# Optimization experiments

Measured on AMD Instinct MI355X. Metric: run time of the kernel, lower is better.

## Reference

```python
import jax, jax.numpy as jnp
import numpy as np

B, T, NUM_SKILLS, CONCEPT_NUM, HIDDEN = 64, 200, 1024, 256, 1024


def setup_inputs() -> dict:
    key = jax.random.key(0)
    ks = jax.random.split(key, 12)
    s_in = 1.0 / np.sqrt(NUM_SKILLS)
    s_h = 1.0 / np.sqrt(HIDDEN)
    s_c = 1.0 / np.sqrt(CONCEPT_NUM)
    return {
        "q_hot": jax.random.normal(ks[0], (B, T, NUM_SKILLS), jnp.float32),
        "result": jax.random.randint(ks[1], (B, T), 0, 2, jnp.int32),
        "next_q_hot": jax.random.normal(ks[2], (B, T, NUM_SKILLS), jnp.float32),
        "concept_num": CONCEPT_NUM,
        # kc: Linear(num_skills -> concept_num)
        "W_kc": jax.random.uniform(ks[3], (CONCEPT_NUM, NUM_SKILLS), jnp.float32, -s_in, s_in),
        "b_kc": jax.random.uniform(ks[4], (CONCEPT_NUM,), jnp.float32, -s_in, s_in),
        # LSTM (input = 2*concept_num, hidden = HIDDEN), torch gate order i,f,g,o
        "W_ih": jax.random.uniform(ks[5], (4 * HIDDEN, 2 * CONCEPT_NUM), jnp.float32, -s_h, s_h),
        "W_hh": jax.random.uniform(ks[6], (4 * HIDDEN, HIDDEN), jnp.float32, -s_h, s_h),
        "b_ih": jax.random.uniform(ks[7], (4 * HIDDEN,), jnp.float32, -s_h, s_h),
        "b_hh": jax.random.uniform(ks[8], (4 * HIDDEN,), jnp.float32, -s_h, s_h),
        # state: Linear(hidden -> concept_num)
        "W_state": jax.random.uniform(ks[9], (CONCEPT_NUM, HIDDEN), jnp.float32, -s_h, s_h),
        "b_state": jax.random.uniform(ks[10], (CONCEPT_NUM,), jnp.float32, -s_h, s_h),
        # out: Linear(concept_num -> 1)
        "W_out": jax.random.uniform(ks[11], (1, CONCEPT_NUM), jnp.float32, -s_c, s_c),
        "b_out": jax.random.uniform(jax.random.fold_in(key, 99), (1,), jnp.float32, -s_c, s_c),
    }


def _lstm(x, W_ih, W_hh, b_ih, b_hh):
    # x: [B, T, In] batch_first; returns h_seq [B, T, H]
    H = W_hh.shape[1]
    xT = jnp.swapaxes(x, 0, 1)                      # [T, B, In]
    gx = jnp.einsum('tbi,gi->tbg', xT, W_ih) + b_ih + b_hh  # [T, B, 4H]
    h0 = jnp.zeros((x.shape[0], H), x.dtype)
    c0 = jnp.zeros((x.shape[0], H), x.dtype)

    def step(carry, g_t):
        h, c = carry
        g = g_t + h @ W_hh.T                        # [B, 4H]
        i, f, gg, o = jnp.split(g, 4, axis=-1)
        i, f, o = jax.nn.sigmoid(i), jax.nn.sigmoid(f), jax.nn.sigmoid(o)
        c = f * c + i * jnp.tanh(gg)
        h = o * jnp.tanh(c)
        return (h, c), h

    _, h_seq = jax.lax.scan(step, (h0, c0), gx)
    return jnp.swapaxes(h_seq, 0, 1)                # [B, T, H]


def reference(q_hot, result, next_q_hot, concept_num,
              W_kc, b_kc, W_ih, W_hh, b_ih, b_hh,
              W_state, b_state, W_out, b_out):
    kc_hot = q_hot @ W_kc.T + b_kc                  # [B, T, C]
    next_kc_hot = next_q_hot @ W_kc.T + b_kc        # [B, T, C]

    # Vectorized replacement of the python double loop:
    # result==1 -> [kc_hot, 0]; else -> [0, kc_hot]
    mask = (result == 1)[..., None].astype(kc_hot.dtype)  # [B, T, 1]
    kc_vec = jnp.concatenate([kc_hot * mask, kc_hot * (1.0 - mask)], axis=-1)  # [B,T,2C]

    h = _lstm(kc_vec, W_ih, W_hh, b_ih, b_hh)       # [B, T, H]
    stu_state = h @ W_state.T + b_state             # [B, T, C]
    knowledge_div = stu_state - next_kc_hot
    vector = knowledge_div * next_kc_hot
    res = vector @ W_out.T + b_out                  # [B, T, 1]
    return (res, stu_state)
```

## Files before the change

kernel.cpp:

```cpp
#include <hip/hip_runtime.h>
#include <math.h>


typedef unsigned short u16;
typedef unsigned long long u64;
typedef __bf16 bf16x8 __attribute__((ext_vector_type(8)));
typedef float floatx4 __attribute__((ext_vector_type(4)));

__device__ __forceinline__ float bf2f(u16 h) {
  unsigned int u = ((unsigned int)h) << 16;
  float f;
  __builtin_memcpy(&f, &u, 4);
  return f;
}
__device__ __forceinline__ u16 f2bf(float f) {
  unsigned int u;
  __builtin_memcpy(&u, &f, 4);
  u += 0x7FFFu + ((u >> 16) & 1u);
  return (u16)(u >> 16);
}
__device__ __forceinline__ float sigm(float x) { return 1.0f / (1.0f + __expf(-x)); }

__global__ void cvt_kernel(const float* __restrict__ in, u16* __restrict__ out) {
  const int i = blockIdx.x * 256 + threadIdx.x;
  const float4 v = ((const float4*)in)[i];
  ushort4 o;
  o.x = f2bf(v.x);
  o.y = f2bf(v.y);
  o.z = f2bf(v.z);
  o.w = f2bf(v.w);
  ((ushort4*)out)[i] = o;
}

template <class Epi>
__global__ __launch_bounds__(256, 2) void gemm_bt(const u16* __restrict__ A,
                                                  const u16* __restrict__ B,
                                                  int M, int N, int K, Epi epi) {
  __shared__ u16 As[128 * 32];
  __shared__ u16 Bs[128 * 32];
  const int tid = threadIdx.x;
  const int w = tid >> 6, lane = tid & 63;
  const int wm = w & 1, wn = w >> 1;
  const int bm = blockIdx.x * 128, bn = blockIdx.y * 128;
  const int lrow = lane & 15, lk8 = (lane >> 4) * 8;
  const int srow = lane >> 2;
  const int skc = (lane & 3) * 8;

  floatx4 acc[4][4] = {};

  for (int k0 = 0; k0 < K; k0 += 32) {
#pragma unroll
    for (int r = 0; r < 2; ++r) {
      const int seg = w * 2 + r;
      const int row = seg * 16 + srow;
      __builtin_amdgcn_global_load_lds(
          (const __attribute__((address_space(1))) unsigned int*)(A + (size_t)(bm + row) * K + k0 + skc),
          (__attribute__((address_space(3))) unsigned int*)(As + seg * 512), 16, 0, 0);
      __builtin_amdgcn_global_load_lds(
          (const __attribute__((address_space(1))) unsigned int*)(B + (size_t)(bn + row) * K + k0 + skc),
          (__attribute__((address_space(3))) unsigned int*)(Bs + seg * 512), 16, 0, 0);
    }
    __syncthreads();

    bf16x8 af[4], bfr[4];
#pragma unroll
    for (int i = 0; i < 4; ++i) {
      af[i] = *(const bf16x8*)(As + (wm * 64 + i * 16 + lrow) * 32 + lk8);
      bfr[i] = *(const bf16x8*)(Bs + (wn * 64 + i * 16 + lrow) * 32 + lk8);
    }
#pragma unroll
    for (int i = 0; i < 4; ++i)
#pragma unroll
      for (int j = 0; j < 4; ++j)
        acc[i][j] = __builtin_amdgcn_mfma_f32_16x16x32_bf16(af[i], bfr[j], acc[i][j], 0, 0, 0);
    __syncthreads();
  }

  const int rbase = bm + wm * 64 + (lane >> 4) * 4;
  const int cbase = bn + wn * 64 + lrow;
#pragma unroll
  for (int i = 0; i < 4; ++i)
#pragma unroll
    for (int j = 0; j < 4; ++j)
#pragma unroll
      for (int r = 0; r < 4; ++r)
        epi(rbase + i * 16 + r, cbase + j * 16, acc[i][j][r]);
}

struct EpiKcVec {
  const float* bkc;
  const int* result;
  u16* kcv;
  __device__ void operator()(int row, int col, float v) const {
    v += bkc[col];
    const int off = (result[row] == 1) ? 0 : 256;
    const size_t base = (size_t)row * 512;
    kcv[base + off + col] = f2bf(v);
    kcv[base + (256 - off) + col] = 0;
  }
};
struct EpiNk {
  const float* bkc;
  float* nk;
  __device__ void operator()(int row, int col, float v) const {
    nk[(size_t)row * 256 + col] = v + bkc[col];
  }
};
struct EpiGx {
  const float* bih;
  const float* bhh;
  u16* gx;
  __device__ void operator()(int row, int col, float v) const {
    v += bih[col] + bhh[col];
    const int b = row / 200, t = row - b * 200;
    gx[(size_t)(t * 64 + b) * 4096 + col] = f2bf(v);
  }
};
struct EpiStu {
  const float* bst;
  float* out;
  __device__ void operator()(int row, int col, float v) const {
    v += bst[col];
    const int b = row & 63, t = row >> 6;
    out[(size_t)(b * 200 + t) * 256 + col] = v;
  }
};

__global__ void init_kernel(u16* hseq, unsigned* flags) {
  const int i = blockIdx.x * 256 + threadIdx.x;
  ((u64*)hseq)[i] = 0ULL;
  if (blockIdx.x == 0) flags[threadIdx.x] = 0u;
}

__global__ __launch_bounds__(256, 1) void lstm_scan(const u16* __restrict__ Whh,
                                                    const u16* __restrict__ gx,
                                                    u16* __restrict__ hseq,
                                                    unsigned* __restrict__ flags) {
  __shared__ __align__(16) u16 Ab[16 * 1032];
  __shared__ float gbuf[4 * 256];
  __shared__ __align__(16) u16 hbuf[256];
  const int tid = threadIdx.x;
  const int w = tid >> 6;
  const int lane = tid & 63;
  const int lrow = lane & 15;
  const int lk8 = (lane >> 4) * 8;
  const int gb = blockIdx.x >> 6;
  const int gn = blockIdx.x & 63;
  const int bb = gb * 16;
  const int j0 = gn * 16;

  bf16x8 bfrag[32];
  {
    const u16* wp = Whh + (size_t)(w * 1024 + j0 + lrow) * 1024 + lk8;
#pragma unroll
    for (int ks = 0; ks < 32; ++ks) bfrag[ks] = *(const bf16x8*)(wp + ks * 32);
  }

  float c_state = 0.0f;
  const int um = tid >> 4, un = tid & 15;

  const u16* gxb = gx + (size_t)(bb + (lane >> 4) * 4) * 4096 + w * 1024 + j0 + lrow;
  u16 gcur[4];
  {
    const u16* gp = gxb;
    gcur[0] = gp[0];
    gcur[1] = gp[4096];
    gcur[2] = gp[8192];
    gcur[3] = gp[12288];
  }

  for (int t = 0; t < 200; ++t) {
    {
      const u64* hs = (const u64*)(hseq + (size_t)t * 65536 + (size_t)bb * 1024);
      u64 tmp[16];
#pragma unroll
      for (int jj = 0; jj < 16; ++jj)
        tmp[jj] = __hip_atomic_load(hs + jj * 256 + tid, __ATOMIC_RELAXED,
                                    __HIP_MEMORY_SCOPE_AGENT);
#pragma unroll
      for (int jj = 0; jj < 16; ++jj) {
        const int ch = jj * 256 + tid;
        const int row = ch >> 8;
        const int cc = (ch & 255) * 4;
        *(u64*)(Ab + row * 1032 + cc) = tmp[jj];
      }
    }
    __syncthreads();

    floatx4 acc;
    acc[0] = bf2f(gcur[0]);
    acc[1] = bf2f(gcur[1]);
    acc[2] = bf2f(gcur[2]);
    acc[3] = bf2f(gcur[3]);
#pragma unroll
    for (int ks = 0; ks < 32; ++ks) {
      bf16x8 a = *(const bf16x8*)(Ab + lrow * 1032 + ks * 32 + lk8);
      acc = __builtin_amdgcn_mfma_f32_16x16x32_bf16(a, bfrag[ks], acc, 0, 0, 0);
    }
    {
      const int mrow = (lane >> 4) * 4;
#pragma unroll
      for (int r = 0; r < 4; ++r) gbuf[w * 256 + (mrow + r) * 16 + lrow] = acc[r];
    }
    __syncthreads();

    const float gi = gbuf[tid];
    const float gf = gbuf[256 + tid];
    const float gg = gbuf[512 + tid];
    const float go = gbuf[768 + tid];
    c_state = sigm(gf) * c_state + sigm(gi) * tanhf(gg);
    const float h = sigm(go) * tanhf(c_state);
    hbuf[um * 16 + un] = f2bf(h);
    __syncthreads();

    if (tid < 64) {
      const int row = lane >> 2, ck = lane & 3;
      const u64 v = *(const u64*)(hbuf + row * 16 + ck * 4);
      u64 old = __hip_atomic_exchange(
          (u64*)(hseq + (size_t)(t + 1) * 65536 + (size_t)(bb + row) * 1024 + j0 + ck * 4),
          v, __ATOMIC_RELAXED, __HIP_MEMORY_SCOPE_AGENT);
      asm volatile("" ::"v"(old));
      asm volatile("s_waitcnt vmcnt(0)" ::: "memory");
      if (lane == 0)
        __hip_atomic_store(&flags[blockIdx.x], (unsigned)(t + 1), __ATOMIC_RELAXED,
                           __HIP_MEMORY_SCOPE_AGENT);
    }

    if (t < 199) {
      const u16* gp = gxb + (size_t)(t + 1) * 64 * 4096;
      gcur[0] = gp[0];
      gcur[1] = gp[4096];
      gcur[2] = gp[8192];
      gcur[3] = gp[12288];
    }

    if (tid < 64) {
      const unsigned tgt = (unsigned)(t + 1);
      const unsigned* gf64 = &flags[gb * 64 + lane];
      for (;;) {
        const unsigned v = __hip_atomic_load(gf64, __ATOMIC_RELAXED,
                                             __HIP_MEMORY_SCOPE_AGENT);
        if (__all(v >= tgt)) break;
        __builtin_amdgcn_s_sleep(1);
      }
    }
    __syncthreads();
  }
}

__global__ void res_kernel(const float* __restrict__ stu, const float* __restrict__ nk,
                           const float* __restrict__ Wout, const float* __restrict__ bout,
                           float* __restrict__ res) {
  const int row = blockIdx.x * 4 + (threadIdx.x >> 6);
  const int lane = threadIdx.x & 63;
  const float* sp = stu + (size_t)row * 256;
  const float* np = nk + (size_t)row * 256;
  float s = 0.0f;
#pragma unroll
  for (int j = 0; j < 4; ++j) {
    const int c = j * 64 + lane;
    const float nv = np[c];
    s += (sp[c] - nv) * nv * Wout[c];
  }
#pragma unroll
  for (int o = 32; o > 0; o >>= 1) s += __shfl_down(s, o, 64);
  if (lane == 0) res[row] = s + bout[0];
}

extern "C" void kernel_launch(void* const* d_in, const int* in_sizes, int n_in,
                              void* d_out, int out_size, void* d_ws, size_t ws_size,
                              hipStream_t stream) {
  const float* q_hot = (const float*)d_in[0];
  const int* result = (const int*)d_in[1];
  const float* next_q = (const float*)d_in[2];
  const float* W_kc = (const float*)d_in[4];
  const float* b_kc = (const float*)d_in[5];
  const float* W_ih = (const float*)d_in[6];
  const float* W_hh = (const float*)d_in[7];
  const float* b_ih = (const float*)d_in[8];
  const float* b_hh = (const float*)d_in[9];
  const float* W_state = (const float*)d_in[10];
  const float* b_state = (const float*)d_in[11];
  const float* W_out = (const float*)d_in[12];
  const float* b_out = (const float*)d_in[13];

  float* out_res = (float*)d_out;
  float* out_stu = out_res + 12800;

  char* ws = (char*)d_ws;
  u16* kcv = (u16*)(ws);
  float* nk = (float*)(ws + 13107200);
  u16* hseq = (u16*)(ws + 26214400);
  u16* Whh_bf = (u16*)(ws + 52559872);
  u16* Wih_bf = (u16*)(ws + 60948480);
  u16* Wkc_bf = (u16*)(ws + 65142784);
  u16* Wst_bf = (u16*)(ws + 65667072);
  unsigned* flags = (unsigned*)(ws + 66191360);
  u16* gx = (u16*)(ws + 66192384);
  u16* q_bf = gx;
  u16* nq_bf = gx + 13107200;

  cvt_kernel<<<dim3(12800), 256, 0, stream>>>(q_hot, q_bf);
  cvt_kernel<<<dim3(12800), 256, 0, stream>>>(next_q, nq_bf);
  cvt_kernel<<<dim3(256), 256, 0, stream>>>(W_kc, Wkc_bf);
  cvt_kernel<<<dim3(2048), 256, 0, stream>>>(W_ih, Wih_bf);
  cvt_kernel<<<dim3(4096), 256, 0, stream>>>(W_hh, Whh_bf);
  cvt_kernel<<<dim3(256), 256, 0, stream>>>(W_state, Wst_bf);

  init_kernel<<<dim3(64), 256, 0, stream>>>(hseq, flags);
  gemm_bt<EpiKcVec><<<dim3(100, 2), 256, 0, stream>>>(q_bf, Wkc_bf, 12800, 256, 1024,
                                                      EpiKcVec{b_kc, result, kcv});
  gemm_bt<EpiNk><<<dim3(100, 2), 256, 0, stream>>>(nq_bf, Wkc_bf, 12800, 256, 1024,
                                                   EpiNk{b_kc, nk});
  gemm_bt<EpiGx><<<dim3(100, 32), 256, 0, stream>>>(kcv, Wih_bf, 12800, 4096, 512,
                                                    EpiGx{b_ih, b_hh, gx});
  lstm_scan<<<dim3(256), 256, 0, stream>>>(Whh_bf, gx, hseq, flags);
  gemm_bt<EpiStu><<<dim3(100, 2), 256, 0, stream>>>(hseq + 65536, Wst_bf, 12800, 256, 1024,
                                                    EpiStu{b_state, out_stu});
  res_kernel<<<dim3(3200), 256, 0, stream>>>(out_stu, nk, W_out, b_out, out_res);
}
```

Measured before the change: 1.331 ms.

## Double-buffer LSTM hidden exchange and let all waves poll flags

```diff
diff --git a/kernel.cpp b/kernel.cpp
--- a/kernel.cpp
+++ b/kernel.cpp
@@ -126,14 +126,15 @@
   }
 };
 
-__global__ void init_kernel(u16* hseq, unsigned* flags) {
+__global__ void init2_kernel(u16* hx, unsigned* flags) {
   const int i = blockIdx.x * 256 + threadIdx.x;
-  ((u64*)hseq)[i] = 0ULL;
+  ((u64*)hx)[i] = 0ULL;
   if (blockIdx.x == 0) flags[threadIdx.x] = 0u;
 }
 
 __global__ __launch_bounds__(256, 1) void lstm_scan(const u16* __restrict__ Whh,
                                                     const u16* __restrict__ gx,
+                                                    u16* __restrict__ hx,
                                                     u16* __restrict__ hseq,
                                                     unsigned* __restrict__ flags) {
   __shared__ __align__(16) u16 Ab[16 * 1032];
@@ -171,15 +172,16 @@
 
   for (int t = 0; t < 200; ++t) {
     {
-      const u64* hs = (const u64*)(hseq + (size_t)t * 65536 + (size_t)bb * 1024);
+      const u64* hs = (const u64*)(hx + (size_t)(t & 1) * 65536 + (size_t)bb * 1024);
       u64 tmp[16];
 #pragma unroll
-      for (int jj = 0; jj < 16; ++jj)
-        tmp[jj] = __hip_atomic_load(hs + jj * 256 + tid, __ATOMIC_RELAXED,
-                                    __HIP_MEMORY_SCOPE_AGENT);
-#pragma unroll
       for (int jj = 0; jj < 16; ++jj) {
-        const int ch = jj * 256 + tid;
+        const int ch = w * 1024 + jj * 64 + lane;
+        tmp[jj] = __hip_atomic_load(hs + ch, __ATOMIC_RELAXED, __HIP_MEMORY_SCOPE_AGENT);
+      }
+#pragma unroll
+      for (int jj = 0; jj < 16; ++jj) {
+        const int ch = w * 1024 + jj * 64 + lane;
         const int row = ch >> 8;
         const int cc = (ch & 255) * 4;
         *(u64*)(Ab + row * 1032 + cc) = tmp[jj];
@@ -216,10 +218,11 @@
     if (tid < 64) {
       const int row = lane >> 2, ck = lane & 3;
       const u64 v = *(const u64*)(hbuf + row * 16 + ck * 4);
-      u64 old = __hip_atomic_exchange(
-          (u64*)(hseq + (size_t)(t + 1) * 65536 + (size_t)(bb + row) * 1024 + j0 + ck * 4),
-          v, __ATOMIC_RELAXED, __HIP_MEMORY_SCOPE_AGENT);
+      const size_t roff = (size_t)(bb + row) * 1024 + j0 + ck * 4;
+      u64 old = __hip_atomic_exchange((u64*)(hx + (size_t)((t + 1) & 1) * 65536 + roff),
+                                      v, __ATOMIC_RELAXED, __HIP_MEMORY_SCOPE_AGENT);
       asm volatile("" ::"v"(old));
+      *(u64*)(hseq + (size_t)(t + 1) * 65536 + roff) = v;
       asm volatile("s_waitcnt vmcnt(0)" ::: "memory");
       if (lane == 0)
         __hip_atomic_store(&flags[blockIdx.x], (unsigned)(t + 1), __ATOMIC_RELAXED,
@@ -234,17 +237,16 @@
       gcur[3] = gp[12288];
     }
 
-    if (tid < 64) {
+    {
       const unsigned tgt = (unsigned)(t + 1);
-      const unsigned* gf64 = &flags[gb * 64 + lane];
+      const unsigned* fp = &flags[gb * 64 + lane];
       for (;;) {
-        const unsigned v = __hip_atomic_load(gf64, __ATOMIC_RELAXED,
+        const unsigned v = __hip_atomic_load(fp, __ATOMIC_RELAXED,
                                              __HIP_MEMORY_SCOPE_AGENT);
         if (__all(v >= tgt)) break;
         __builtin_amdgcn_s_sleep(1);
       }
     }
-    __syncthreads();
   }
 }
 
@@ -289,6 +291,7 @@
 
   char* ws = (char*)d_ws;
   u16* kcv = (u16*)(ws);
+  u16* hx = kcv;
   float* nk = (float*)(ws + 13107200);
   u16* hseq = (u16*)(ws + 26214400);
   u16* Whh_bf = (u16*)(ws + 52559872);
@@ -307,14 +310,14 @@
   cvt_kernel<<<dim3(4096), 256, 0, stream>>>(W_hh, Whh_bf);
   cvt_kernel<<<dim3(256), 256, 0, stream>>>(W_state, Wst_bf);
 
-  init_kernel<<<dim3(64), 256, 0, stream>>>(hseq, flags);
   gemm_bt<EpiKcVec><<<dim3(100, 2), 256, 0, stream>>>(q_bf, Wkc_bf, 12800, 256, 1024,
                                                       EpiKcVec{b_kc, result, kcv});
   gemm_bt<EpiNk><<<dim3(100, 2), 256, 0, stream>>>(nq_bf, Wkc_bf, 12800, 256, 1024,
                                                    EpiNk{b_kc, nk});
   gemm_bt<EpiGx><<<dim3(100, 32), 256, 0, stream>>>(kcv, Wih_bf, 12800, 4096, 512,
                                                     EpiGx{b_ih, b_hh, gx});
-  lstm_scan<<<dim3(256), 256, 0, stream>>>(Whh_bf, gx, hseq, flags);
+  init2_kernel<<<dim3(128), 256, 0, stream>>>(hx, flags);
+  lstm_scan<<<dim3(256), 256, 0, stream>>>(Whh_bf, gx, hx, hseq, flags);
   gemm_bt<EpiStu><<<dim3(100, 2), 256, 0, stream>>>(hseq + 65536, Wst_bf, 12800, 256, 1024,
                                                     EpiStu{b_state, out_stu});
   res_kernel<<<dim3(3200), 256, 0, stream>>>(out_stu, nk, W_out, b_out, out_res);
```

After: 1.588 ms. +19.3%, slower.
